# Kernel optimization log

Hardware: AMD Instinct MI355X
Metric: run time of the kernel (lower is better)

The kernel has to match this reference:

```python
import jax, jax.numpy as jnp
import numpy as np

B, T = 65536, 100          # batch of trajectories, hard-coded 100-step unrolled loop
D_CP, D_FIN, HID, D_OUT = 2, 3, 12, 2  # control-point dim, finger dim, SimpleRNN units, Dense out


def setup_inputs() -> dict:
    key = jax.random.key(0)
    k0, k1, k2, k3, k4 = jax.random.split(key, 5)
    return {
        "control_point_input": jax.random.normal(k0, (B, T, D_CP), jnp.float32),
        "finger_input": jax.random.normal(k1, (B, T, D_FIN), jnp.float32),
        # SimpleRNN kernel / recurrent kernel / bias ('random_normal', 'zeros')
        "W_rnn": jax.random.normal(k2, (D_CP + D_FIN, HID), jnp.float32) * 0.05,
        "U_rnn": jax.random.normal(k3, (HID, HID), jnp.float32) * 0.05,
        "b_rnn": jnp.zeros((HID,), jnp.float32),
        # Dense(2) kernel / bias
        "W_out": jax.random.normal(k4, (D_CP + HID, D_OUT), jnp.float32) * 0.05,
        "b_out": jnp.zeros((D_OUT,), jnp.float32),
    }


def reference(control_point_input, finger_input, W_rnn, U_rnn, b_rnn, W_out, b_out):
    """Non-teacher-forcing branch of DeformationTrackerBiFlowModel.call.

    Keras SimpleRNN (stateful=False) is invoked on a single timestep each
    iteration, so its hidden state is reset to zero every call and the
    recurrent kernel U_rnn contributes h0 @ U_rnn == 0 (mathematically inert).
    The true autoregressive recurrence flows through the Dense(2) output fed
    back as the next step's input -> expressed with a single lax.scan.
    """
    cp0 = control_point_input[:, 0, :]                # (B, 2), reused at every step
    fin = jnp.transpose(finger_input, (1, 0, 2))      # (T, B, 3) for scan

    def step(prev_out, fin_t):
        # prev_out: (B, 2) previous predicted control point; fin_t: (B, 3)
        x = jnp.concatenate([prev_out, fin_t], axis=-1)          # (B, 5)
        h = jnp.tanh(x @ W_rnn + b_rnn)                          # (B, 12); h0 @ U_rnn == 0
        out = jnp.concatenate([cp0, h], axis=-1) @ W_out + b_out  # (B, 2)
        return out, out

    _, outs = jax.lax.scan(step, cp0, fin)            # outs: (T, B, 2)
    return jnp.transpose(outs, (1, 0, 2))             # (B, T, 2)
```

## Files before the change

kernel.cpp:

```cpp
#include <hip/hip_runtime.h>


constexpr int Bn  = 65536;
constexpr int Tn  = 100;
constexpr int HID = 12;

__device__ __forceinline__ float fast_tanh(float a) {
    const float ax = __builtin_fabsf(a);
    const float t  = __builtin_amdgcn_exp2f(ax * -2.885390081777927f);
    const float r  = (1.0f - t) * __builtin_amdgcn_rcpf(1.0f + t);
    return __builtin_copysignf(r, a);
}

__global__ __launch_bounds__(256, 1) void deform_kernel(
    const float* __restrict__ cp,
    const float* __restrict__ fin,
    const float* __restrict__ Wr,
    const float* __restrict__ br_,
    const float* __restrict__ Wo,
    const float* __restrict__ bo_,
    float* __restrict__ out)
{
    const int b = blockIdx.x * blockDim.x + threadIdx.x;

    float w[5][HID];
    #pragma unroll
    for (int i = 0; i < 5; ++i)
        #pragma unroll
        for (int j = 0; j < HID; ++j)
            w[i][j] = Wr[i * HID + j];

    float br[HID];
    #pragma unroll
    for (int j = 0; j < HID; ++j) br[j] = br_[j];

    float woh[HID][2];
    #pragma unroll
    for (int j = 0; j < HID; ++j) {
        woh[j][0] = Wo[(2 + j) * 2 + 0];
        woh[j][1] = Wo[(2 + j) * 2 + 1];
    }
    const float wo00 = Wo[0], wo01 = Wo[1];
    const float wo10 = Wo[2], wo11 = Wo[3];
    const float bo0 = bo_[0], bo1 = bo_[1];

    const float cp0x = cp[(size_t)b * Tn * 2 + 0];
    const float cp0y = cp[(size_t)b * Tn * 2 + 1];

    const float oc0 = bo0 + cp0x * wo00 + cp0y * wo10;
    const float oc1 = bo1 + cp0x * wo01 + cp0y * wo11;

    float px = cp0x, py = cp0y;

    const float4* __restrict__ fp = reinterpret_cast<const float4*>(fin + (size_t)b * Tn * 3);
    float4* __restrict__ op = reinterpret_cast<float4*>(out + (size_t)b * Tn * 2);

    float4 cur0 = fp[0], cur1 = fp[1], cur2 = fp[2];
    float4 nxt0 = fp[3], nxt1 = fp[4], nxt2 = fp[5];

    #pragma unroll 1
    for (int c = 0; c < 25; ++c) {
        const int cpre = (c + 2 < 25) ? (c + 2) : 24;
        const float4 pf0 = fp[cpre * 3 + 0];
        const float4 pf1 = fp[cpre * 3 + 1];
        const float4 pf2 = fp[cpre * 3 + 2];

        const float f[12] = {cur0.x, cur0.y, cur0.z, cur0.w,
                             cur1.x, cur1.y, cur1.z, cur1.w,
                             cur2.x, cur2.y, cur2.z, cur2.w};
        float o[8];
        #pragma unroll
        for (int s = 0; s < 4; ++s) {
            const float fx = f[s * 3 + 0];
            const float fy = f[s * 3 + 1];
            const float fz = f[s * 3 + 2];
            float o0 = oc0, o1 = oc1;
            #pragma unroll
            for (int j = 0; j < HID; ++j) {
                const float a = br[j] + px * w[0][j] + py * w[1][j]
                              + fx * w[2][j] + fy * w[3][j] + fz * w[4][j];
                const float h = fast_tanh(a);
                o0 += h * woh[j][0];
                o1 += h * woh[j][1];
            }
            o[s * 2 + 0] = o0;
            o[s * 2 + 1] = o1;
            px = o0; py = o1;
        }

        op[c * 2 + 0] = make_float4(o[0], o[1], o[2], o[3]);
        op[c * 2 + 1] = make_float4(o[4], o[5], o[6], o[7]);

        cur0 = nxt0; cur1 = nxt1; cur2 = nxt2;
        nxt0 = pf0;  nxt1 = pf1;  nxt2 = pf2;
    }
}

extern "C" void kernel_launch(void* const* d_in, const int* in_sizes, int n_in,
                              void* d_out, int out_size, void* d_ws, size_t ws_size,
                              hipStream_t stream) {
    const float* cp  = (const float*)d_in[0];
    const float* fin = (const float*)d_in[1];
    const float* Wr  = (const float*)d_in[2];
    const float* br  = (const float*)d_in[4];
    const float* Wo  = (const float*)d_in[5];
    const float* bo  = (const float*)d_in[6];
    float* out = (float*)d_out;

    deform_kernel<<<dim3(Bn / 256), dim3(256), 0, stream>>>(cp, fin, Wr, br, Wo, bo, out);
}
```

Baseline: 222.8 us.

## Split hidden units across four lanes per trajectory with DPP reductions

Each trajectory is now handled by four lanes, each computing three of the twelve hidden units. Partial output sums are combined with DPP quad shuffles, and each lane writes one float2 per chunk. The launch uses four times as many threads, and the tanh is simplified to one exp and one reciprocal. The aim is to shorten each lane's serial dependency chain and raise occupancy. The cost is redundant finger-input loads in all four lanes, shuffle latency on every step, and narrower output stores.

```diff
diff --git a/kernel.cpp b/kernel.cpp
--- a/kernel.cpp
+++ b/kernel.cpp
@@ -4,15 +4,21 @@
 constexpr int Bn  = 65536;
 constexpr int Tn  = 100;
 constexpr int HID = 12;
+constexpr int LPR = 4;
+constexpr int UPL = 3;
+
+template <int CTRL>
+__device__ __forceinline__ float dpp_mov(float x) {
+    return __builtin_bit_cast(float,
+        __builtin_amdgcn_mov_dpp(__builtin_bit_cast(int, x), CTRL, 0xF, 0xF, true));
+}
 
 __device__ __forceinline__ float fast_tanh(float a) {
-    const float ax = __builtin_fabsf(a);
-    const float t  = __builtin_amdgcn_exp2f(ax * -2.885390081777927f);
-    const float r  = (1.0f - t) * __builtin_amdgcn_rcpf(1.0f + t);
-    return __builtin_copysignf(r, a);
+    const float t = __builtin_amdgcn_exp2f(a * 2.885390081777927f);
+    return __builtin_fmaf(-2.0f, __builtin_amdgcn_rcpf(1.0f + t), 1.0f);
 }
 
-__global__ __launch_bounds__(256, 1) void deform_kernel(
+__global__ __launch_bounds__(256, 4) void deform_kernel(
     const float* __restrict__ cp,
     const float* __restrict__ fin,
     const float* __restrict__ Wr,
@@ -21,39 +27,39 @@
     const float* __restrict__ bo_,
     float* __restrict__ out)
 {
-    const int b = blockIdx.x * blockDim.x + threadIdx.x;
+    const int tid = blockIdx.x * blockDim.x + threadIdx.x;
+    const int row = tid >> 2;
+    const int q   = tid & 3;
+    const int j0  = q * UPL;
 
-    float w[5][HID];
+    float w0[UPL], w1[UPL], w2[UPL], w3[UPL], w4[UPL];
+    float brv[UPL], wo0[UPL], wo1[UPL];
     #pragma unroll
-    for (int i = 0; i < 5; ++i)
-        #pragma unroll
-        for (int j = 0; j < HID; ++j)
-            w[i][j] = Wr[i * HID + j];
-
-    float br[HID];
-    #pragma unroll
-    for (int j = 0; j < HID; ++j) br[j] = br_[j];
-
-    float woh[HID][2];
-    #pragma unroll
-    for (int j = 0; j < HID; ++j) {
-        woh[j][0] = Wo[(2 + j) * 2 + 0];
-        woh[j][1] = Wo[(2 + j) * 2 + 1];
+    for (int u = 0; u < UPL; ++u) {
+        const int j = j0 + u;
+        w0[u] = Wr[0 * HID + j];
+        w1[u] = Wr[1 * HID + j];
+        w2[u] = Wr[2 * HID + j];
+        w3[u] = Wr[3 * HID + j];
+        w4[u] = Wr[4 * HID + j];
+        brv[u] = br_[j];
+        wo0[u] = Wo[(2 + j) * 2 + 0];
+        wo1[u] = Wo[(2 + j) * 2 + 1];
     }
     const float wo00 = Wo[0], wo01 = Wo[1];
     const float wo10 = Wo[2], wo11 = Wo[3];
     const float bo0 = bo_[0], bo1 = bo_[1];
 
-    const float cp0x = cp[(size_t)b * Tn * 2 + 0];
-    const float cp0y = cp[(size_t)b * Tn * 2 + 1];
+    const float cp0x = cp[(size_t)row * Tn * 2 + 0];
+    const float cp0y = cp[(size_t)row * Tn * 2 + 1];
 
     const float oc0 = bo0 + cp0x * wo00 + cp0y * wo10;
     const float oc1 = bo1 + cp0x * wo01 + cp0y * wo11;
 
     float px = cp0x, py = cp0y;
 
-    const float4* __restrict__ fp = reinterpret_cast<const float4*>(fin + (size_t)b * Tn * 3);
-    float4* __restrict__ op = reinterpret_cast<float4*>(out + (size_t)b * Tn * 2);
+    const float4* __restrict__ fp = reinterpret_cast<const float4*>(fin + (size_t)row * Tn * 3);
+    float2* __restrict__ op = reinterpret_cast<float2*>(out + (size_t)row * Tn * 2);
 
     float4 cur0 = fp[0], cur1 = fp[1], cur2 = fp[2];
     float4 nxt0 = fp[3], nxt1 = fp[4], nxt2 = fp[5];
@@ -68,28 +74,38 @@
         const float f[12] = {cur0.x, cur0.y, cur0.z, cur0.w,
                              cur1.x, cur1.y, cur1.z, cur1.w,
                              cur2.x, cur2.y, cur2.z, cur2.w};
-        float o[8];
+
+        float so0 = 0.0f, so1 = 0.0f;
         #pragma unroll
         for (int s = 0; s < 4; ++s) {
             const float fx = f[s * 3 + 0];
             const float fy = f[s * 3 + 1];
             const float fz = f[s * 3 + 2];
-            float o0 = oc0, o1 = oc1;
+            float o0p = 0.0f, o1p = 0.0f;
             #pragma unroll
-            for (int j = 0; j < HID; ++j) {
-                const float a = br[j] + px * w[0][j] + py * w[1][j]
-                              + fx * w[2][j] + fy * w[3][j] + fz * w[4][j];
+            for (int u = 0; u < UPL; ++u) {
+                float a = brv[u];
+                a = __builtin_fmaf(px, w0[u], a);
+                a = __builtin_fmaf(py, w1[u], a);
+                a = __builtin_fmaf(fx, w2[u], a);
+                a = __builtin_fmaf(fy, w3[u], a);
+                a = __builtin_fmaf(fz, w4[u], a);
                 const float h = fast_tanh(a);
-                o0 += h * woh[j][0];
-                o1 += h * woh[j][1];
+                o0p = __builtin_fmaf(h, wo0[u], o0p);
+                o1p = __builtin_fmaf(h, wo1[u], o1p);
             }
-            o[s * 2 + 0] = o0;
-            o[s * 2 + 1] = o1;
+            o0p += dpp_mov<0xB1>(o0p);
+            o1p += dpp_mov<0xB1>(o1p);
+            o0p += dpp_mov<0x4E>(o0p);
+            o1p += dpp_mov<0x4E>(o1p);
+
+            const float o0 = oc0 + o0p;
+            const float o1 = oc1 + o1p;
+            if (q == s) { so0 = o0; so1 = o1; }
             px = o0; py = o1;
         }
 
-        op[c * 2 + 0] = make_float4(o[0], o[1], o[2], o[3]);
-        op[c * 2 + 1] = make_float4(o[4], o[5], o[6], o[7]);
+        op[c * 4 + q] = make_float2(so0, so1);
 
         cur0 = nxt0; cur1 = nxt1; cur2 = nxt2;
         nxt0 = pf0;  nxt1 = pf1;  nxt2 = pf2;
@@ -107,5 +123,6 @@
     const float* bo  = (const float*)d_in[6];
     float* out = (float*)d_out;
 
-    deform_kernel<<<dim3(Bn / 256), dim3(256), 0, stream>>>(cp, fin, Wr, br, Wo, bo, out);
+    const int threads = Bn * LPR;
+    deform_kernel<<<dim3(threads / 256), dim3(256), 0, stream>>>(cp, fin, Wr, br, Wo, bo, out);
 }
```

New measurement: 210.3 us. -5.6%, faster.

## Stage finger inputs and outputs through LDS for coalesced global access

Applied to the files above, without the earlier changes.

Global loads and stores are now done cooperatively by the block in 20-timestep windows: finger data is loaded with coalesced float4 reads into padded shared memory, each thread runs its recurrence from LDS, and outputs are staged in LDS and written back coalesced. The previous version had each thread stride through its own row, so a wavefront's accesses were scattered. The tanh is rewritten with fewer instructions (1 - 2/(1+e^{2a})) and the hidden-unit math is rebuilt as explicit FMA chains. The cost is block-wide barriers between the load, compute and store phases, with no overlap between memory and compute inside a block, plus extra LDS use (about 105 KB) that limits residency to one block per CU. The new tanh form could also be less accurate for large |a|, where exp2 can overflow to inf.

```diff
diff --git a/kernel.cpp b/kernel.cpp
--- a/kernel.cpp
+++ b/kernel.cpp
@@ -1,15 +1,18 @@
 #include <hip/hip_runtime.h>
 
 
-constexpr int Bn  = 65536;
-constexpr int Tn  = 100;
-constexpr int HID = 12;
+constexpr int Bn   = 65536;
+constexpr int Tn   = 100;
+constexpr int HID  = 12;
+constexpr int ROWS = 256;
+constexpr int W    = 20;
+constexpr int NW   = Tn / W;
+constexpr int FS   = 61;
+constexpr int OS   = 42;
 
 __device__ __forceinline__ float fast_tanh(float a) {
-    const float ax = __builtin_fabsf(a);
-    const float t  = __builtin_amdgcn_exp2f(ax * -2.885390081777927f);
-    const float r  = (1.0f - t) * __builtin_amdgcn_rcpf(1.0f + t);
-    return __builtin_copysignf(r, a);
+    const float t = __builtin_amdgcn_exp2f(a * 2.885390081777927f);
+    return __builtin_fmaf(-2.0f, __builtin_amdgcn_rcpf(1.0f + t), 1.0f);
 }
 
 __global__ __launch_bounds__(256, 1) void deform_kernel(
@@ -21,78 +24,106 @@
     const float* __restrict__ bo_,
     float* __restrict__ out)
 {
-    const int b = blockIdx.x * blockDim.x + threadIdx.x;
+    __shared__ float fin_lds[ROWS * FS];
+    __shared__ float out_lds[ROWS * OS];
 
-    float w[5][HID];
-    #pragma unroll
-    for (int i = 0; i < 5; ++i)
-        #pragma unroll
-        for (int j = 0; j < HID; ++j)
-            w[i][j] = Wr[i * HID + j];
+    const int t  = threadIdx.x;
+    const int r0 = blockIdx.x * ROWS;
 
-    float br[HID];
-    #pragma unroll
-    for (int j = 0; j < HID; ++j) br[j] = br_[j];
-
-    float woh[HID][2];
+    float w0[HID], w1[HID], w2[HID], w3[HID], w4[HID];
+    float brv[HID], wo0[HID], wo1[HID];
     #pragma unroll
     for (int j = 0; j < HID; ++j) {
-        woh[j][0] = Wo[(2 + j) * 2 + 0];
-        woh[j][1] = Wo[(2 + j) * 2 + 1];
+        w0[j] = Wr[0 * HID + j];
+        w1[j] = Wr[1 * HID + j];
+        w2[j] = Wr[2 * HID + j];
+        w3[j] = Wr[3 * HID + j];
+        w4[j] = Wr[4 * HID + j];
+        brv[j] = br_[j];
+        wo0[j] = Wo[(2 + j) * 2 + 0];
+        wo1[j] = Wo[(2 + j) * 2 + 1];
     }
     const float wo00 = Wo[0], wo01 = Wo[1];
     const float wo10 = Wo[2], wo11 = Wo[3];
     const float bo0 = bo_[0], bo1 = bo_[1];
 
-    const float cp0x = cp[(size_t)b * Tn * 2 + 0];
-    const float cp0y = cp[(size_t)b * Tn * 2 + 1];
+    const float cx = cp[(size_t)(r0 + t) * (Tn * 2) + 0];
+    const float cy = cp[(size_t)(r0 + t) * (Tn * 2) + 1];
+    const float oc0 = bo0 + cx * wo00 + cy * wo10;
+    const float oc1 = bo1 + cx * wo01 + cy * wo11;
 
-    const float oc0 = bo0 + cp0x * wo00 + cp0y * wo10;
-    const float oc1 = bo1 + cp0x * wo01 + cp0y * wo11;
+    float px = cx, py = cy;
 
-    float px = cp0x, py = cp0y;
-
-    const float4* __restrict__ fp = reinterpret_cast<const float4*>(fin + (size_t)b * Tn * 3);
-    float4* __restrict__ op = reinterpret_cast<float4*>(out + (size_t)b * Tn * 2);
-
-    float4 cur0 = fp[0], cur1 = fp[1], cur2 = fp[2];
-    float4 nxt0 = fp[3], nxt1 = fp[4], nxt2 = fp[5];
+    const float4* __restrict__ fin4 = reinterpret_cast<const float4*>(fin);
+    float4* __restrict__ out4 = reinterpret_cast<float4*>(out);
 
     #pragma unroll 1
-    for (int c = 0; c < 25; ++c) {
-        const int cpre = (c + 2 < 25) ? (c + 2) : 24;
-        const float4 pf0 = fp[cpre * 3 + 0];
-        const float4 pf1 = fp[cpre * 3 + 1];
-        const float4 pf2 = fp[cpre * 3 + 2];
+    for (int w = 0; w < NW; ++w) {
+        float4 v[15];
+        #pragma unroll
+        for (int k = 0; k < 15; ++k) {
+            const int q   = t + k * 256;
+            const int row = q / 15;
+            const int p4  = q % 15;
+            v[k] = fin4[(size_t)(r0 + row) * 75 + w * 15 + p4];
+        }
+        #pragma unroll
+        for (int k = 0; k < 15; ++k) {
+            const int q   = t + k * 256;
+            const int row = q / 15;
+            const int p4  = q % 15;
+            float* dst = &fin_lds[row * FS + p4 * 4];
+            dst[0] = v[k].x; dst[1] = v[k].y; dst[2] = v[k].z; dst[3] = v[k].w;
+        }
+        __syncthreads();
 
-        const float f[12] = {cur0.x, cur0.y, cur0.z, cur0.w,
-                             cur1.x, cur1.y, cur1.z, cur1.w,
-                             cur2.x, cur2.y, cur2.z, cur2.w};
-        float o[8];
+        {
+            const int fb = t * FS;
+            float f0 = fin_lds[fb + 0];
+            float f1 = fin_lds[fb + 1];
+            float f2 = fin_lds[fb + 2];
+            #pragma unroll 1
+            for (int s = 0; s < W; ++s) {
+                float nf0 = 0.f, nf1 = 0.f, nf2 = 0.f;
+                if (s + 1 < W) {
+                    nf0 = fin_lds[fb + 3 * (s + 1) + 0];
+                    nf1 = fin_lds[fb + 3 * (s + 1) + 1];
+                    nf2 = fin_lds[fb + 3 * (s + 1) + 2];
+                }
+                float o0p = 0.f, o1p = 0.f;
+                #pragma unroll
+                for (int j = 0; j < HID; ++j) {
+                    const float g = __builtin_fmaf(f2, w4[j],
+                                    __builtin_fmaf(f1, w3[j],
+                                    __builtin_fmaf(f0, w2[j], brv[j])));
+                    const float a = __builtin_fmaf(py, w1[j],
+                                    __builtin_fmaf(px, w0[j], g));
+                    const float h = fast_tanh(a);
+                    o0p = __builtin_fmaf(h, wo0[j], o0p);
+                    o1p = __builtin_fmaf(h, wo1[j], o1p);
+                }
+                const float o0 = oc0 + o0p;
+                const float o1 = oc1 + o1p;
+                px = o0; py = o1;
+                *reinterpret_cast<float2*>(&out_lds[t * OS + 2 * s]) =
+                    make_float2(o0, o1);
+                f0 = nf0; f1 = nf1; f2 = nf2;
+            }
+        }
+        __syncthreads();
+
         #pragma unroll
-        for (int s = 0; s < 4; ++s) {
-            const float fx = f[s * 3 + 0];
-            const float fy = f[s * 3 + 1];
-            const float fz = f[s * 3 + 2];
-            float o0 = oc0, o1 = oc1;
-            #pragma unroll
-            for (int j = 0; j < HID; ++j) {
-                const float a = br[j] + px * w[0][j] + py * w[1][j]
-                              + fx * w[2][j] + fy * w[3][j] + fz * w[4][j];
-                const float h = fast_tanh(a);
-                o0 += h * woh[j][0];
-                o1 += h * woh[j][1];
-            }
-            o[s * 2 + 0] = o0;
-            o[s * 2 + 1] = o1;
-            px = o0; py = o1;
+        for (int k = 0; k < 10; ++k) {
+            const int q   = t + k * 256;
+            const int row = q / 10;
+            const int p4  = q % 10;
+            const float2* s2 =
+                reinterpret_cast<const float2*>(&out_lds[row * OS + p4 * 4]);
+            const float2 a0 = s2[0];
+            const float2 a1 = s2[1];
+            out4[(size_t)(r0 + row) * 50 + w * 10 + p4] =
+                make_float4(a0.x, a0.y, a1.x, a1.y);
         }
-
-        op[c * 2 + 0] = make_float4(o[0], o[1], o[2], o[3]);
-        op[c * 2 + 1] = make_float4(o[4], o[5], o[6], o[7]);
-
-        cur0 = nxt0; cur1 = nxt1; cur2 = nxt2;
-        nxt0 = pf0;  nxt1 = pf1;  nxt2 = pf2;
     }
 }
 
@@ -107,5 +138,5 @@
     const float* bo  = (const float*)d_in[6];
     float* out = (float*)d_out;
 
-    deform_kernel<<<dim3(Bn / 256), dim3(256), 0, stream>>>(cp, fin, Wr, br, Wo, bo, out);
+    deform_kernel<<<dim3(Bn / ROWS), dim3(ROWS), 0, stream>>>(cp, fin, Wr, br, Wo, bo, out);
 }
```

New measurement: 219.7 us. Within noise of the previous version (-1.4%).
